# Kernel optimization log

Hardware: AMD Instinct MI355X
Metric: run time of the kernel (lower is better)

Reference implementation:

```python
import jax, jax.numpy as jnp
import numpy as np

B, L = 256, 256
TAU = 0.01


def setup_inputs() -> dict:
    key = jax.random.key(0)
    k1, k2, k3, k4 = jax.random.split(key, 4)
    x = jax.random.normal(k1, (B, L, B), dtype=jnp.float32)
    target = jax.random.normal(k2, (B, L, B), dtype=jnp.float32)
    mask = jnp.ones((B, L), dtype=jnp.int32)  # prefix-valid mask per query; all clips valid
    query_labels = jax.random.randint(k3, (B,), 0, B, dtype=jnp.int64)
    label_mat = jax.random.randint(k4, (B, B), 0, 2, dtype=jnp.int32)  # label_dict[i] -> row i
    return {"x": x, "target": target, "mask": mask, "query_labels": query_labels, "label_mat": label_mat}


def reference(x, target, mask, query_labels, label_mat):
    # x, target: [B, L, B] (batch, clips, queries); mask: [B(queries), L]
    xs = jax.nn.softmax(x, axis=1)
    ts = jax.nn.softmax(target, axis=1)
    m = (mask > 0).astype(xs.dtype)  # [i(query), l]
    # mask target clips per query i (equivalent to the original's :m prefix slice
    # because mask is a contiguous prefix of valid clips)
    tsm = ts * m.T[None, :, :]  # [c, l, i]
    # sim[i, b, c] = sum_l xs[b, l, i] * ts[c, l, i] * m[i, l]  (per-query B x B matmul)
    sim = jnp.einsum('bli,cli->ibc', xs, tsm)
    logits = sim / TAU
    # original computes -log(exp(n_ji)/sum_c exp(n_jc)) == -log_softmax over c, picked at class i
    logp = jax.nn.log_softmax(logits, axis=-1)  # [i, j, c]
    per = jnp.diagonal(logp, axis1=0, axis2=2)  # per[j, i] = logp[i, j, i]
    loss = -(label_mat.astype(xs.dtype).T * per).sum() / x.shape[0]
    return loss
```

## Files before the change

kernel.cpp:

```cpp
#include <hip/hip_runtime.h>
#include <hip/hip_bf16.h>

#define NB 256
#define NL 256
#define SCALE 100.0f

typedef __attribute__((ext_vector_type(4))) unsigned int u32x4;
typedef __attribute__((ext_vector_type(8))) __bf16 bfrag8;
typedef __attribute__((ext_vector_type(4))) float f32x4;

static __device__ __forceinline__ unsigned int pack2bf(float a, float b) {
  union { float f; unsigned int u; } ua, ub;
  ua.f = a; ub.f = b;
  unsigned int ra = (ua.u + 0x7FFFu + ((ua.u >> 16) & 1u)) >> 16;
  unsigned int rb = (ub.u + 0x7FFFu + ((ub.u >> 16) & 1u)) & 0xFFFF0000u;
  return ra | rb;
}

__global__ __launch_bounds__(1024, 2) void exp_t(
    const float* __restrict__ x, const float* __restrict__ tgt,
    unsigned int* __restrict__ xsT, unsigned int* __restrict__ tsT,
    float* __restrict__ sumx, float* __restrict__ sumt)
{
  const int b = blockIdx.x;
  const bool is_t = (blockIdx.y != 0);
  const int tid = threadIdx.x;
  const int i = tid & 255;
  const int h = tid >> 8;
  const float* src = (is_t ? tgt : x) + (size_t)b * (NL * NB) + i;
  unsigned int* dstb = (is_t ? tsT : xsT);

  __shared__ __align__(16) unsigned char stg[256 * 128];
  __shared__ float s_sum[4][256];

  const int r0 = tid >> 3;
  const int c  = tid & 7;

  float tsum = 0.f;

  for (int lc = 0; lc < 4; ++lc) {
    float v[16];
    #pragma unroll
    for (int k = 0; k < 16; ++k)
      v[k] = __expf(src[(size_t)(lc * 64 + h * 16 + k) * NB]);
    #pragma unroll
    for (int k = 0; k < 16; ++k) tsum += v[k];
    u32x4 p0, p1;
    p0.x = pack2bf(v[0], v[1]);   p0.y = pack2bf(v[2], v[3]);
    p0.z = pack2bf(v[4], v[5]);   p0.w = pack2bf(v[6], v[7]);
    p1.x = pack2bf(v[8], v[9]);   p1.y = pack2bf(v[10], v[11]);
    p1.z = pack2bf(v[12], v[13]); p1.w = pack2bf(v[14], v[15]);
    *reinterpret_cast<u32x4*>(&stg[i * 128 + (((h * 2 + 0) ^ (i & 7)) << 4)]) = p0;
    *reinterpret_cast<u32x4*>(&stg[i * 128 + (((h * 2 + 1) ^ (i & 7)) << 4)]) = p1;
    __syncthreads();
    u32x4 q0 = *reinterpret_cast<const u32x4*>(&stg[r0 * 128 + ((c ^ (r0 & 7)) << 4)]);
    u32x4 q1 = *reinterpret_cast<const u32x4*>(&stg[(r0 + 128) * 128 + ((c ^ ((r0 + 128) & 7)) << 4)]);
    *reinterpret_cast<u32x4*>(dstb + ((size_t)b * 256 + r0) * 128 + lc * 32 + c * 4) = q0;
    *reinterpret_cast<u32x4*>(dstb + ((size_t)b * 256 + r0 + 128) * 128 + lc * 32 + c * 4) = q1;
    __syncthreads();
  }

  s_sum[h][i] = tsum;
  __syncthreads();
  if (h == 0) {
    float* so = is_t ? sumt : sumx;
    so[(size_t)b * 256 + i] = s_sum[0][i] + s_sum[1][i] + s_sum[2][i] + s_sum[3][i];
  }
}

__global__ __launch_bounds__(256, 2) void gemm_lse(
    const unsigned short* __restrict__ xsT,
    const unsigned short* __restrict__ tsT,
    const float* __restrict__ sumx,
    const float* __restrict__ sumt,
    const int* __restrict__ mask,
    const int* __restrict__ label_mat,
    float* __restrict__ out)
{
  const int n  = blockIdx.x;
  const int g  = n & 7;
  const int q  = n >> 3;
  const int i  = ((q >> 2) << 3) + g;
  const int jt = q & 3;
  const int t  = threadIdx.x;
  const int w  = t >> 6;
  const int lane = t & 63;

  __shared__ __align__(16) unsigned char As[64 * 128];
  __shared__ __align__(16) unsigned char Bs[256 * 128];
  __shared__ __align__(16) unsigned short s_mask[NL];
  __shared__ float s_irx[64];
  __shared__ float s_ict[256];
  __shared__ float s_rmax[4][64];
  __shared__ float s_rsum[4][64];
  __shared__ float s_diag[64];

  const int srow = t >> 3;
  const int sch  = t & 7;

  f32x4 acc[4][4];
  #pragma unroll
  for (int a = 0; a < 4; ++a)
    #pragma unroll
    for (int cc = 0; cc < 4; ++cc) acc[a][cc] = f32x4{0.f, 0.f, 0.f, 0.f};

  u32x4 areg[2], breg[8];

  auto load_chunk = [&](int kc) {
    const int kofs = kc * 64;
    #pragma unroll
    for (int r = 0; r < 2; ++r) {
      int row = srow + r * 32;
      areg[r] = *reinterpret_cast<const u32x4*>(
          xsT + ((size_t)(jt * 64 + row) * 256 + i) * 256 + kofs + sch * 8);
    }
    #pragma unroll
    for (int r = 0; r < 8; ++r) {
      int row = srow + r * 32;
      breg[r] = *reinterpret_cast<const u32x4*>(
          tsT + ((size_t)row * 256 + i) * 256 + kofs + sch * 8);
    }
  };
  auto store_chunk = [&](int kc) {
    u32x4 mk = *reinterpret_cast<const u32x4*>(&s_mask[kc * 64 + sch * 8]);
    #pragma unroll
    for (int r = 0; r < 2; ++r) {
      int row = srow + r * 32;
      *reinterpret_cast<u32x4*>(&As[row * 128 + ((sch ^ (row & 7)) << 4)]) = areg[r];
    }
    #pragma unroll
    for (int r = 0; r < 8; ++r) {
      int row = srow + r * 32;
      u32x4 bm = breg[r];
      bm.x &= mk.x; bm.y &= mk.y; bm.z &= mk.z; bm.w &= mk.w;
      *reinterpret_cast<u32x4*>(&Bs[row * 128 + ((sch ^ (row & 7)) << 4)]) = bm;
    }
  };

  load_chunk(0);
  s_mask[t] = (mask[i * NL + t] > 0) ? (unsigned short)0xFFFFu : (unsigned short)0u;
  s_ict[t] = __builtin_amdgcn_rcpf(sumt[(size_t)t * 256 + i]);
  if (t < 64)
    s_irx[t] = SCALE * __builtin_amdgcn_rcpf(sumx[(size_t)(jt * 64 + t) * 256 + i]);
  __syncthreads();

  #pragma unroll
  for (int kc = 0; kc < 4; ++kc) {
    store_chunk(kc);
    __syncthreads();
    if (kc < 3) load_chunk(kc + 1);
    #pragma unroll
    for (int kk = 0; kk < 2; ++kk) {
      const int co = kk * 4 + (lane >> 4);
      bfrag8 af[4], bfr[4];
      #pragma unroll
      for (int jf = 0; jf < 4; ++jf) {
        int row = jf * 16 + (lane & 15);
        af[jf] = *reinterpret_cast<const bfrag8*>(
            &As[row * 128 + ((co ^ (row & 7)) << 4)]);
      }
      #pragma unroll
      for (int cf = 0; cf < 4; ++cf) {
        int row = w * 64 + cf * 16 + (lane & 15);
        bfr[cf] = *reinterpret_cast<const bfrag8*>(
            &Bs[row * 128 + ((co ^ (row & 7)) << 4)]);
      }
      #pragma unroll
      for (int jf = 0; jf < 4; ++jf)
        #pragma unroll
        for (int cf = 0; cf < 4; ++cf)
          acc[jf][cf] = __builtin_amdgcn_mfma_f32_16x16x32_bf16(
              af[jf], bfr[cf], acc[jf][cf], 0, 0, 0);
    }
    __syncthreads();
  }

  const int rg = (lane >> 4) << 2;

  float fr[4][4], fc[4];
  #pragma unroll
  for (int jf = 0; jf < 4; ++jf)
    #pragma unroll
    for (int reg = 0; reg < 4; ++reg)
      fr[jf][reg] = s_irx[jf * 16 + rg + reg];
  #pragma unroll
  for (int cf = 0; cf < 4; ++cf)
    fc[cf] = s_ict[w * 64 + cf * 16 + (lane & 15)];
  #pragma unroll
  for (int jf = 0; jf < 4; ++jf)
    #pragma unroll
    for (int cf = 0; cf < 4; ++cf)
      #pragma unroll
      for (int reg = 0; reg < 4; ++reg)
        acc[jf][cf][reg] *= fr[jf][reg] * fc[cf];

  #pragma unroll
  for (int jf = 0; jf < 4; ++jf) {
    #pragma unroll
    for (int reg = 0; reg < 4; ++reg) {
      float m = fmaxf(fmaxf(acc[jf][0][reg], acc[jf][1][reg]),
                      fmaxf(acc[jf][2][reg], acc[jf][3][reg]));
      #pragma unroll
      for (int off = 1; off < 16; off <<= 1) m = fmaxf(m, __shfl_xor(m, off, 64));
      if ((lane & 15) == 0) s_rmax[w][jf * 16 + rg + reg] = m;
    }
  }
  if (w == (i >> 6) && (lane & 15) == (i & 15)) {
    const int cfd = (i >> 4) & 3;
    #pragma unroll
    for (int jf = 0; jf < 4; ++jf) {
      #pragma unroll
      for (int reg = 0; reg < 4; ++reg) {
        float v = acc[jf][0][reg];
        #pragma unroll
        for (int cf = 1; cf < 4; ++cf)
          v = (cfd == cf) ? acc[jf][cf][reg] : v;
        s_diag[jf * 16 + rg + reg] = v;
      }
    }
  }
  __syncthreads();

  #pragma unroll
  for (int jf = 0; jf < 4; ++jf) {
    #pragma unroll
    for (int reg = 0; reg < 4; ++reg) {
      int row = jf * 16 + rg + reg;
      float gm = fmaxf(fmaxf(s_rmax[0][row], s_rmax[1][row]),
                       fmaxf(s_rmax[2][row], s_rmax[3][row]));
      float sE = 0.f;
      #pragma unroll
      for (int cf = 0; cf < 4; ++cf) sE += __expf(acc[jf][cf][reg] - gm);
      #pragma unroll
      for (int off = 1; off < 16; off <<= 1) sE += __shfl_xor(sE, off, 64);
      if ((lane & 15) == 0) s_rsum[w][row] = sE;
    }
  }
  __syncthreads();

  float contrib = 0.f;
  if (t < 64) {
    const int row = t;
    float gm = fmaxf(fmaxf(s_rmax[0][row], s_rmax[1][row]),
                     fmaxf(s_rmax[2][row], s_rmax[3][row]));
    float tot = s_rsum[0][row] + s_rsum[1][row] + s_rsum[2][row] + s_rsum[3][row];
    float lse = __logf(tot) + gm;
    float lbl = (float)label_mat[i * NB + jt * 64 + row];
    contrib = lbl * (s_diag[row] - lse);
  }
  #pragma unroll
  for (int off = 32; off >= 1; off >>= 1) contrib += __shfl_down(contrib, off, 64);
  if (t == 0) atomicAdd(out, contrib * (-1.0f / 256.0f));
}

extern "C" void kernel_launch(void* const* d_in, const int* in_sizes, int n_in,
                              void* d_out, int out_size, void* d_ws, size_t ws_size,
                              hipStream_t stream) {
  const float* x   = (const float*)d_in[0];
  const float* tgt = (const float*)d_in[1];
  const int* mask  = (const int*)d_in[2];
  const int* label_mat = (const int*)d_in[4];
  float* out = (float*)d_out;

  unsigned int* xsT = (unsigned int*)d_ws;
  unsigned int* tsT = xsT + (size_t)NB * NB * NL / 2;
  float* sumx = (float*)(tsT + (size_t)NB * NB * NL / 2);
  float* sumt = sumx + (size_t)NB * NB;

  hipMemsetAsync(out, 0, sizeof(float), stream);
  exp_t<<<dim3(NB, 2), 1024, 0, stream>>>(x, tgt, xsT, tsT, sumx, sumt);
  gemm_lse<<<dim3(1024), 256, 0, stream>>>((const unsigned short*)xsT,
                                           (const unsigned short*)tsT,
                                           sumx, sumt, mask, label_mat, out);
}
```

Baseline: 75.73 us.

## Vectorize exp-transpose loads and split L across blocks with atomic sums

Restructures the exp/transpose kernel so each thread loads float4 vectors along the query dimension instead of scalar loads, and splits the clip dimension across two blocks per batch (grid z) with 512 threads each. Column sums are now combined with atomicAdd into buffers zeroed by an extra memset. The aim is wider global loads, more blocks in flight, and higher occupancy for the bandwidth-bound softmax preprocessing. The cost is an extra memset launch and atomic traffic, plus a changed LDS swizzle pattern.

```diff
diff --git a/kernel.cpp b/kernel.cpp
--- a/kernel.cpp
+++ b/kernel.cpp
@@ -17,54 +17,71 @@
   return ra | rb;
 }
 
-__global__ __launch_bounds__(1024, 2) void exp_t(
+__global__ __launch_bounds__(512, 8) void exp_t(
     const float* __restrict__ x, const float* __restrict__ tgt,
     unsigned int* __restrict__ xsT, unsigned int* __restrict__ tsT,
     float* __restrict__ sumx, float* __restrict__ sumt)
 {
-  const int b = blockIdx.x;
+  const int b  = blockIdx.x;
   const bool is_t = (blockIdx.y != 0);
+  const int z  = blockIdx.z;
   const int tid = threadIdx.x;
-  const int i = tid & 255;
-  const int h = tid >> 8;
-  const float* src = (is_t ? tgt : x) + (size_t)b * (NL * NB) + i;
+  const int i4 = tid & 63;
+  const int lg = tid >> 6;
+  const f32x4* src4 = reinterpret_cast<const f32x4*>(
+      (is_t ? tgt : x) + (size_t)b * (NL * NB));
   unsigned int* dstb = (is_t ? tsT : xsT);
 
   __shared__ __align__(16) unsigned char stg[256 * 128];
-  __shared__ float s_sum[4][256];
-
-  const int r0 = tid >> 3;
-  const int c  = tid & 7;
-
-  float tsum = 0.f;
-
-  for (int lc = 0; lc < 4; ++lc) {
-    float v[16];
-    #pragma unroll
-    for (int k = 0; k < 16; ++k)
-      v[k] = __expf(src[(size_t)(lc * 64 + h * 16 + k) * NB]);
-    #pragma unroll
-    for (int k = 0; k < 16; ++k) tsum += v[k];
-    u32x4 p0, p1;
-    p0.x = pack2bf(v[0], v[1]);   p0.y = pack2bf(v[2], v[3]);
-    p0.z = pack2bf(v[4], v[5]);   p0.w = pack2bf(v[6], v[7]);
-    p1.x = pack2bf(v[8], v[9]);   p1.y = pack2bf(v[10], v[11]);
-    p1.z = pack2bf(v[12], v[13]); p1.w = pack2bf(v[14], v[15]);
-    *reinterpret_cast<u32x4*>(&stg[i * 128 + (((h * 2 + 0) ^ (i & 7)) << 4)]) = p0;
-    *reinterpret_cast<u32x4*>(&stg[i * 128 + (((h * 2 + 1) ^ (i & 7)) << 4)]) = p1;
+  __shared__ float s_ps[8][256];
+
+  float psum[4] = {0.f, 0.f, 0.f, 0.f};
+
+  #pragma unroll
+  for (int r = 0; r < 2; ++r) {
+    const int lbase = z * 128 + r * 64;
+    f32x4 rv[8];
+    #pragma unroll
+    for (int k = 0; k < 8; ++k)
+      rv[k] = src4[(size_t)(lbase + lg * 8 + k) * 64 + i4];
+    #pragma unroll
+    for (int ii = 0; ii < 4; ++ii) {
+      float e[8];
+      #pragma unroll
+      for (int k = 0; k < 8; ++k) {
+        e[k] = __expf(rv[k][ii]);
+        psum[ii] += e[k];
+      }
+      u32x4 pk;
+      pk.x = pack2bf(e[0], e[1]);
+      pk.y = pack2bf(e[2], e[3]);
+      pk.z = pack2bf(e[4], e[5]);
+      pk.w = pack2bf(e[6], e[7]);
+      const int row = i4 * 4 + ii;
+      const int ch  = lg ^ (i4 & 7);
+      *reinterpret_cast<u32x4*>(&stg[row * 128 + (ch << 4)]) = pk;
+    }
     __syncthreads();
-    u32x4 q0 = *reinterpret_cast<const u32x4*>(&stg[r0 * 128 + ((c ^ (r0 & 7)) << 4)]);
-    u32x4 q1 = *reinterpret_cast<const u32x4*>(&stg[(r0 + 128) * 128 + ((c ^ ((r0 + 128) & 7)) << 4)]);
-    *reinterpret_cast<u32x4*>(dstb + ((size_t)b * 256 + r0) * 128 + lc * 32 + c * 4) = q0;
-    *reinterpret_cast<u32x4*>(dstb + ((size_t)b * 256 + r0 + 128) * 128 + lc * 32 + c * 4) = q1;
-    __syncthreads();
-  }
-
-  s_sum[h][i] = tsum;
-  __syncthreads();
-  if (h == 0) {
-    float* so = is_t ? sumt : sumx;
-    so[(size_t)b * 256 + i] = s_sum[0][i] + s_sum[1][i] + s_sum[2][i] + s_sum[3][i];
+    const int c = tid & 7;
+    #pragma unroll
+    for (int k = 0; k < 4; ++k) {
+      const int row = (tid >> 3) + 64 * k;
+      const int cp  = c ^ ((row >> 2) & 7);
+      u32x4 q = *reinterpret_cast<const u32x4*>(&stg[row * 128 + (cp << 4)]);
+      *reinterpret_cast<u32x4*>(
+          dstb + ((size_t)b * 256 + row) * 128 + z * 64 + r * 32 + c * 4) = q;
+    }
+    if (r == 0) __syncthreads();
+  }
+
+  #pragma unroll
+  for (int ii = 0; ii < 4; ++ii) s_ps[lg][i4 * 4 + ii] = psum[ii];
+  __syncthreads();
+  if (tid < 256) {
+    float tot = 0.f;
+    #pragma unroll
+    for (int k = 0; k < 8; ++k) tot += s_ps[k][tid];
+    atomicAdd((is_t ? sumt : sumx) + (size_t)b * 256 + tid, tot);
   }
 }
 
@@ -268,7 +285,8 @@
   float* sumt = sumx + (size_t)NB * NB;
 
   hipMemsetAsync(out, 0, sizeof(float), stream);
-  exp_t<<<dim3(NB, 2), 1024, 0, stream>>>(x, tgt, xsT, tsT, sumx, sumt);
+  hipMemsetAsync(sumx, 0, 2 * (size_t)NB * NB * sizeof(float), stream);
+  exp_t<<<dim3(NB, 2, 2), 512, 0, stream>>>(x, tgt, xsT, tsT, sumx, sumt);
   gemm_lse<<<dim3(1024), 256, 0, stream>>>((const unsigned short*)xsT,
                                            (const unsigned short*)tsT,
                                            sumx, sumt, mask, label_mat, out);
```

Result: slower. 86.03 us (+13.6%).
